# Optimization experiments

Measured on AMD Instinct MI355X. Metric: run time of the kernel, lower is better.

## Reference

```python
import jax, jax.numpy as jnp
import numpy as np

B, S, D = 4, 4096, 768

def setup_inputs() -> dict:
    key = jax.random.key(0)
    k1, k2, k3, k4 = jax.random.split(key, 4)
    x = jax.random.normal(k1, (B, S, D), dtype=jnp.float32)
    # nn.Linear weights: shape [d_out, d_in], applied as x @ W.T
    scale = 1.0 / np.sqrt(D)
    Wq = jax.random.normal(k2, (D, D), dtype=jnp.float32) * scale
    Wk = jax.random.normal(k3, (D, D), dtype=jnp.float32) * scale
    Wv = jax.random.normal(k4, (D, D), dtype=jnp.float32) * scale
    return {"x": x, "Wq": Wq, "Wk": Wk, "Wv": Wv}

def reference(x, Wq, Wk, Wv):
    b, s, d = x.shape
    q = jnp.einsum('bsd,ed->bse', x, Wq)  # Linear: x @ W.T
    k = jnp.einsum('bsd,ed->bse', x, Wk)
    v = jnp.einsum('bsd,ed->bse', x, Wv)
    scores = jnp.einsum('bqe,bke->bqk', q, k)  # [B,S,S]
    causal = jnp.triu(jnp.ones((s, s), dtype=bool), k=1)
    scores = jnp.where(causal, -jnp.inf, scores)
    # original scales by d_out**0.5 (full dim, single head)
    attn = jax.nn.softmax(scores / jnp.sqrt(jnp.asarray(d, x.dtype)), axis=-1)
    return jnp.einsum('bqk,bke->bqe', attn, v)
```

## Files before the change

### kernel.cpp

```cpp
#include <hip/hip_runtime.h>
#include <hip/hip_fp16.h>

typedef unsigned short u16;
typedef unsigned int   u32;
typedef __attribute__((ext_vector_type(8))) _Float16 f16x8;
typedef __attribute__((ext_vector_type(4))) float    f32x4;

#define MFMA(a,b,c) __builtin_amdgcn_mfma_f32_16x16x32_f16(a,b,c,0,0,0)

__device__ __forceinline__ u16 f2h(float f) { return __half_as_ushort(__float2half(f)); }

__device__ __forceinline__ void load_lds16(const void* g, void* l) {
    __builtin_amdgcn_global_load_lds(
        (__attribute__((address_space(1))) void*)g,
        (__attribute__((address_space(3))) void*)l,
        16, 0, 0);
}

__global__ __launch_bounds__(256) void k_conv_x(const float* __restrict__ in, u16* __restrict__ out)
{
    int i = blockIdx.x * 256 + threadIdx.x;
    float4 v = ((const float4*)in)[i];
    ushort4 o; o.x = f2h(v.x); o.y = f2h(v.y); o.z = f2h(v.z); o.w = f2h(v.w);
    ((ushort4*)out)[i] = o;
}

__global__ __launch_bounds__(256) void k_conv_w(const float* __restrict__ w0, const float* __restrict__ w1,
                                                const float* __restrict__ w2, u16* __restrict__ out)
{
    const float* src = (blockIdx.y == 0) ? w0 : (blockIdx.y == 1) ? w1 : w2;
    int i = blockIdx.x * 256 + threadIdx.x;
    float4 v = ((const float4*)src)[i];
    ushort4 o; o.x = f2h(v.x); o.y = f2h(v.y); o.z = f2h(v.z); o.w = f2h(v.w);
    ((ushort4*)(out + (size_t)blockIdx.y * 589824))[i] = o;
}

__global__ __launch_bounds__(256) void k_gemm(const u16* __restrict__ xb, const u16* __restrict__ Wb,
                                              u16* __restrict__ Qw, u16* __restrict__ Kw, u16* __restrict__ Vt)
{
    __shared__ u16 As[2][128*32];
    __shared__ u16 Bs[2][128*32];
    const int tid = threadIdx.x;
    const int l = tid & 63;
    const int wr = tid >> 7, wc = (tid >> 6) & 1;
    const int z = blockIdx.z, bx = blockIdx.x;
    const u16 *Ap, *Bp; u16* Cp; int m0, n0; size_t ldc;
    if (z < 2) { Ap = xb; Bp = Wb + (size_t)z*589824; Cp = (z==0)?Qw:Kw; m0=(bx/6)*128; n0=(bx%6)*128; ldc=768; }
    else       { Ap = Wb + 2*589824; Bp = xb; Cp = Vt; m0=(bx%6)*128; n0=(bx/6)*128; ldc=16384; }

    f32x4 acc[4][4];
    #pragma unroll
    for (int i=0;i<4;++i)
        #pragma unroll
        for (int j=0;j<4;++j) acc[i][j] = (f32x4){0.f,0.f,0.f,0.f};

    const int srow = tid >> 2, sg = tid & 3;
    const int wb = (tid >> 6) << 10;

    #pragma unroll
    for (int i = 0; i < 2; ++i) {
        load_lds16(Ap + (size_t)(m0 + i*64 + srow)*768 + sg*8, (char*)&As[0][0] + i*4096 + wb);
        load_lds16(Bp + (size_t)(n0 + i*64 + srow)*768 + sg*8, (char*)&Bs[0][0] + i*4096 + wb);
    }
    __syncthreads();
    int cur = 0;
    for (int kt = 0; kt < 24; ++kt) {
        if (kt + 1 < 24) {
            const int k0 = (kt+1)*32;
            #pragma unroll
            for (int i = 0; i < 2; ++i) {
                load_lds16(Ap + (size_t)(m0 + i*64 + srow)*768 + k0 + sg*8, (char*)&As[cur^1][0] + i*4096 + wb);
                load_lds16(Bp + (size_t)(n0 + i*64 + srow)*768 + k0 + sg*8, (char*)&Bs[cur^1][0] + i*4096 + wb);
            }
        }
        f16x8 a[4], b[4];
        #pragma unroll
        for (int mi = 0; mi < 4; ++mi) a[mi] = *(const f16x8*)&As[cur][(wr*64 + mi*16 + (l&15))*32 + (l>>4)*8];
        #pragma unroll
        for (int ni = 0; ni < 4; ++ni) b[ni] = *(const f16x8*)&Bs[cur][(wc*64 + ni*16 + (l&15))*32 + (l>>4)*8];
        #pragma unroll
        for (int mi = 0; mi < 4; ++mi)
            #pragma unroll
            for (int ni = 0; ni < 4; ++ni)
                acc[mi][ni] = MFMA(a[mi], b[ni], acc[mi][ni]);
        __syncthreads();
        cur ^= 1;
    }
    const int col = l & 15, rg = (l >> 4) * 4;
    #pragma unroll
    for (int mi = 0; mi < 4; ++mi)
        #pragma unroll
        for (int ni = 0; ni < 4; ++ni)
            #pragma unroll
            for (int j = 0; j < 4; ++j)
                Cp[(size_t)(m0 + wr*64 + mi*16 + rg + j) * ldc + n0 + wc*64 + ni*16 + col] = f2h(acc[mi][ni][j]);
}

#define SM_SCALE 0.03608439182435161f

__global__ __launch_bounds__(1024, 4) void k_flash(const u16* __restrict__ Qg, const u16* __restrict__ Kg,
                                                   const u16* __restrict__ Vtg, float* __restrict__ Og)
{
    __shared__ u16 Qs[32*768];
    __shared__ u16 Ks[32*768];
    __shared__ float Sp[4][32][34];
    __shared__ u16 Ps[32][40];
    __shared__ float row_m[32], row_l[32], row_sc[32];

    const int tid = threadIdx.x;
    const int w = tid >> 6, l = tid & 63;
    const int l15 = l & 15, l4 = l >> 4;
    const int iq = w & 1, jk = (w >> 1) & 1, kh = w >> 2;
    const int dg = w;
    const int batch = blockIdx.x & 3, p = blockIdx.x >> 2;
    const size_t bofs = (size_t)batch * 4096;
    const float NEG_INF = -__builtin_inff();
    const int wbase = w << 10;

    for (int pass = 0; pass < 2; ++pass) {
        const int qi = pass ? p : 127 - p;
        const int q0 = qi * 32;
        const int NT = qi + 1;

        if (tid < 32) { row_m[tid] = NEG_INF; row_l[tid] = 0.f; }

        #pragma unroll
        for (int i = 0; i < 3; ++i) {
            int u = i*1024 + tid, row = u/96, g = u - row*96, gd = g ^ (row & 7);
            load_lds16(Qg + (bofs + q0 + row)*768 + gd*8, (char*)Qs + i*16384 + wbase);
        }
        #pragma unroll
        for (int i = 0; i < 3; ++i) {
            int u = i*1024 + tid, row = u/96, g = u - row*96, gd = g ^ (row & 7);
            load_lds16(Kg + (bofs + row)*768 + gd*8, (char*)Ks + i*16384 + wbase);
        }

        f32x4 oacc[2][3];
        #pragma unroll
        for (int a = 0; a < 2; ++a)
            #pragma unroll
            for (int b = 0; b < 3; ++b) oacc[a][b] = (f32x4){0.f,0.f,0.f,0.f};
        f16x8 vfr[3];

        for (int t = 0; t < NT; ++t) {
            __syncthreads();
            {
                const int qrow = iq*16 + l15, krow = jk*16 + l15;
                const char* qb = (const char*)Qs + qrow*1536;
                const char* kb = (const char*)Ks + krow*1536;
                const int qx = qrow & 7, kx = krow & 7;
                f32x4 s0 = (f32x4){0.f,0.f,0.f,0.f}, s1 = (f32x4){0.f,0.f,0.f,0.f};
                #pragma unroll
                for (int s = 0; s < 6; s += 2) {
                    const int g0 = kh*24 + s*4 + l4, g1 = g0 + 4;
                    f16x8 a0 = *(const f16x8*)(qb + (g0 ^ qx)*16);
                    f16x8 b0 = *(const f16x8*)(kb + (g0 ^ kx)*16);
                    s0 = MFMA(a0, b0, s0);
                    f16x8 a1 = *(const f16x8*)(qb + (g1 ^ qx)*16);
                    f16x8 b1 = *(const f16x8*)(kb + (g1 ^ kx)*16);
                    s1 = MFMA(a1, b1, s1);
                }
                const int sr = iq*16 + l4*4, scc = jk*16 + l15;
                #pragma unroll
                for (int j = 0; j < 4; ++j)
                    Sp[kh][sr + j][scc] = s0[j] + s1[j];
            }
            if (t > 0) {
                const int rb = l4*4;
                #pragma unroll
                for (int qg = 0; qg < 2; ++qg) {
                    const float fr0 = row_sc[qg*16+rb],   fr1 = row_sc[qg*16+rb+1],
                                fr2 = row_sc[qg*16+rb+2], fr3 = row_sc[qg*16+rb+3];
                    f16x8 pa = *(const f16x8*)((const char*)&Ps[0][0] + (qg*16 + l15)*80 + l4*16);
                    #pragma unroll
                    for (int ni = 0; ni < 3; ++ni) {
                        f32x4 o = oacc[qg][ni];
                        o[0]*=fr0; o[1]*=fr1; o[2]*=fr2; o[3]*=fr3;
                        oacc[qg][ni] = MFMA(pa, vfr[ni], o);
                    }
                }
            }
            __syncthreads();
            if (t + 1 < NT) {
                #pragma unroll
                for (int i = 0; i < 3; ++i) {
                    int u = i*1024 + tid, row = u/96, g = u - row*96, gd = g ^ (row & 7);
                    load_lds16(Kg + (bofs + (t+1)*32 + row)*768 + gd*8, (char*)Ks + i*16384 + wbase);
                }
            }
            {
                const u16* vb = Vtg + (size_t)(dg*48 + l15)*16384 + bofs + t*32 + l4*8;
                #pragma unroll
                for (int ni = 0; ni < 3; ++ni)
                    vfr[ni] = *(const f16x8*)(vb + (size_t)ni*262144);
            }
            {
                const int r = tid >> 5, c = tid & 31;
                float a = (Sp[0][r][c] + Sp[1][r][c] + Sp[2][r][c] + Sp[3][r][c]) * SM_SCALE;
                const int qglob = q0 + r, kglob = t*32 + c;
                if (kglob > qglob) a = NEG_INF;
                float mx = a;
                mx = fmaxf(mx, __shfl_xor(mx, 1));
                mx = fmaxf(mx, __shfl_xor(mx, 2));
                mx = fmaxf(mx, __shfl_xor(mx, 4));
                mx = fmaxf(mx, __shfl_xor(mx, 8));
                mx = fmaxf(mx, __shfl_xor(mx, 16));
                const float m_old = row_m[r];
                const float m_new = fmaxf(m_old, mx);
                const float pr = __expf(a - m_new);
                float sum = pr;
                sum += __shfl_xor(sum, 1);
                sum += __shfl_xor(sum, 2);
                sum += __shfl_xor(sum, 4);
                sum += __shfl_xor(sum, 8);
                sum += __shfl_xor(sum, 16);
                const float sc = __expf(m_old - m_new);
                if (c == 0) { row_m[r] = m_new; row_l[r] = row_l[r]*sc + sum; row_sc[r] = sc; }
                Ps[r][c] = f2h(pr);
            }
        }
        __syncthreads();
        {
            const int rb = l4*4;
            #pragma unroll
            for (int qg = 0; qg < 2; ++qg) {
                const float fr0 = row_sc[qg*16+rb],   fr1 = row_sc[qg*16+rb+1],
                            fr2 = row_sc[qg*16+rb+2], fr3 = row_sc[qg*16+rb+3];
                f16x8 pa = *(const f16x8*)((const char*)&Ps[0][0] + (qg*16 + l15)*80 + l4*16);
                #pragma unroll
                for (int ni = 0; ni < 3; ++ni) {
                    f32x4 o = oacc[qg][ni];
                    o[0]*=fr0; o[1]*=fr1; o[2]*=fr2; o[3]*=fr3;
                    oacc[qg][ni] = MFMA(pa, vfr[ni], o);
                }
            }
        }
        {
            const int rb = l4*4;
            #pragma unroll
            for (int qg = 0; qg < 2; ++qg) {
                const float i0 = 1.f/row_l[qg*16+rb],   i1 = 1.f/row_l[qg*16+rb+1],
                            i2 = 1.f/row_l[qg*16+rb+2], i3 = 1.f/row_l[qg*16+rb+3];
                #pragma unroll
                for (int ni = 0; ni < 3; ++ni) {
                    const size_t base = (bofs + q0 + qg*16 + rb) * 768 + dg*48 + ni*16 + l15;
                    Og[base]        = oacc[qg][ni][0] * i0;
                    Og[base + 768]  = oacc[qg][ni][1] * i1;
                    Og[base + 1536] = oacc[qg][ni][2] * i2;
                    Og[base + 2304] = oacc[qg][ni][3] * i3;
                }
            }
        }
        __syncthreads();
    }
}

extern "C" void kernel_launch(void* const* d_in, const int* in_sizes, int n_in,
                              void* d_out, int out_size, void* d_ws, size_t ws_size,
                              hipStream_t stream)
{
    const float* x  = (const float*)d_in[0];
    const float* Wq = (const float*)d_in[1];
    const float* Wk = (const float*)d_in[2];
    const float* Wv = (const float*)d_in[3];
    float* out = (float*)d_out;
    char* ws = (char*)d_ws;
    u16* xb = (u16*)ws;
    u16* Wb = (u16*)(ws + 25165824);
    u16* Qw = (u16*)(ws + 28704768);
    u16* Kw = (u16*)(ws + 53870592);
    u16* Vt = (u16*)(ws + 79036416);

    k_conv_x<<<12288, 256, 0, stream>>>(x, xb);
    k_conv_w<<<dim3(576, 3), 256, 0, stream>>>(Wq, Wk, Wv, Wb);
    k_gemm<<<dim3(768, 1, 3), 256, 0, stream>>>(xb, Wb, Qw, Kw, Vt);
    k_flash<<<256, 1024, 0, stream>>>(Qw, Kw, Vt, out);
}
```

Before: 515.9 us.

## Widen flash attention key tile to 64 and keep Q fragments in registers

Doubles the key/value tile per iteration from 32 to 64 rows, which halves the number of loop iterations and block-wide barriers per query tile. Q is now held in registers, loaded once per pass, instead of being staged in LDS, which frees shared memory for the larger K buffer. The softmax step handles two columns per thread with vectorized LDS reads and writes. The cost is higher register pressure from the Q and doubled V fragments, and more LDS per block, which may reduce occupancy.

```diff
diff --git a/kernel.cpp b/kernel.cpp
--- a/kernel.cpp
+++ b/kernel.cpp
@@ -101,16 +101,15 @@
 __global__ __launch_bounds__(1024, 4) void k_flash(const u16* __restrict__ Qg, const u16* __restrict__ Kg,
                                                    const u16* __restrict__ Vtg, float* __restrict__ Og)
 {
-    __shared__ u16 Qs[32*768];
-    __shared__ u16 Ks[32*768];
-    __shared__ float Sp[4][32][34];
-    __shared__ u16 Ps[32][40];
+    __shared__ u16 Ks[64*768];
+    __shared__ float Sp[4][32][66];
+    __shared__ u16 Ps[32][72];
     __shared__ float row_m[32], row_l[32], row_sc[32];
 
     const int tid = threadIdx.x;
     const int w = tid >> 6, l = tid & 63;
     const int l15 = l & 15, l4 = l >> 4;
-    const int iq = w & 1, jk = (w >> 1) & 1, kh = w >> 2;
+    const int jk = w & 3, kh = w >> 2;
     const int dg = w;
     const int batch = blockIdx.x & 3, p = blockIdx.x >> 2;
     const size_t bofs = (size_t)batch * 4096;
@@ -120,17 +119,21 @@
     for (int pass = 0; pass < 2; ++pass) {
         const int qi = pass ? p : 127 - p;
         const int q0 = qi * 32;
-        const int NT = qi + 1;
+        const int NT = (qi >> 1) + 1;
 
         if (tid < 32) { row_m[tid] = NEG_INF; row_l[tid] = 0.f; }
 
-        #pragma unroll
-        for (int i = 0; i < 3; ++i) {
-            int u = i*1024 + tid, row = u/96, g = u - row*96, gd = g ^ (row & 7);
-            load_lds16(Qg + (bofs + q0 + row)*768 + gd*8, (char*)Qs + i*16384 + wbase);
-        }
-        #pragma unroll
-        for (int i = 0; i < 3; ++i) {
+        f16x8 qf[2][6];
+        {
+            const u16* qb = Qg + (bofs + q0 + l15)*768 + kh*192 + l4*8;
+            #pragma unroll
+            for (int iq = 0; iq < 2; ++iq)
+                #pragma unroll
+                for (int ks = 0; ks < 6; ++ks)
+                    qf[iq][ks] = *(const f16x8*)(qb + iq*12288 + ks*32);
+        }
+        #pragma unroll
+        for (int i = 0; i < 6; ++i) {
             int u = i*1024 + tid, row = u/96, g = u - row*96, gd = g ^ (row & 7);
             load_lds16(Kg + (bofs + row)*768 + gd*8, (char*)Ks + i*16384 + wbase);
         }
@@ -140,30 +143,27 @@
         for (int a = 0; a < 2; ++a)
             #pragma unroll
             for (int b = 0; b < 3; ++b) oacc[a][b] = (f32x4){0.f,0.f,0.f,0.f};
-        f16x8 vfr[3];
+        f16x8 vfr[2][3];
 
         for (int t = 0; t < NT; ++t) {
             __syncthreads();
             {
-                const int qrow = iq*16 + l15, krow = jk*16 + l15;
-                const char* qb = (const char*)Qs + qrow*1536;
-                const char* kb = (const char*)Ks + krow*1536;
-                const int qx = qrow & 7, kx = krow & 7;
+                const char* kb = (const char*)Ks + (jk*16 + l15)*1536;
+                const int kx = l15 & 7;
                 f32x4 s0 = (f32x4){0.f,0.f,0.f,0.f}, s1 = (f32x4){0.f,0.f,0.f,0.f};
                 #pragma unroll
-                for (int s = 0; s < 6; s += 2) {
-                    const int g0 = kh*24 + s*4 + l4, g1 = g0 + 4;
-                    f16x8 a0 = *(const f16x8*)(qb + (g0 ^ qx)*16);
-                    f16x8 b0 = *(const f16x8*)(kb + (g0 ^ kx)*16);
-                    s0 = MFMA(a0, b0, s0);
-                    f16x8 a1 = *(const f16x8*)(qb + (g1 ^ qx)*16);
-                    f16x8 b1 = *(const f16x8*)(kb + (g1 ^ kx)*16);
-                    s1 = MFMA(a1, b1, s1);
-                }
-                const int sr = iq*16 + l4*4, scc = jk*16 + l15;
-                #pragma unroll
-                for (int j = 0; j < 4; ++j)
-                    Sp[kh][sr + j][scc] = s0[j] + s1[j];
+                for (int ks = 0; ks < 6; ++ks) {
+                    const int g = kh*24 + ks*4 + l4;
+                    f16x8 bk = *(const f16x8*)(kb + (g ^ kx)*16);
+                    s0 = MFMA(qf[0][ks], bk, s0);
+                    s1 = MFMA(qf[1][ks], bk, s1);
+                }
+                const int scc = jk*16 + l15, sr = l4*4;
+                #pragma unroll
+                for (int j = 0; j < 4; ++j) {
+                    Sp[kh][sr + j][scc]      = s0[j];
+                    Sp[kh][16 + sr + j][scc] = s1[j];
+                }
             }
             if (t > 0) {
                 const int rb = l4*4;
@@ -171,35 +171,46 @@
                 for (int qg = 0; qg < 2; ++qg) {
                     const float fr0 = row_sc[qg*16+rb],   fr1 = row_sc[qg*16+rb+1],
                                 fr2 = row_sc[qg*16+rb+2], fr3 = row_sc[qg*16+rb+3];
-                    f16x8 pa = *(const f16x8*)((const char*)&Ps[0][0] + (qg*16 + l15)*80 + l4*16);
+                    f16x8 pa0 = *(const f16x8*)((const char*)&Ps[0][0] + (qg*16 + l15)*144 + l4*16);
+                    f16x8 pa1 = *(const f16x8*)((const char*)&Ps[0][0] + (qg*16 + l15)*144 + 64 + l4*16);
                     #pragma unroll
                     for (int ni = 0; ni < 3; ++ni) {
                         f32x4 o = oacc[qg][ni];
                         o[0]*=fr0; o[1]*=fr1; o[2]*=fr2; o[3]*=fr3;
-                        oacc[qg][ni] = MFMA(pa, vfr[ni], o);
+                        o = MFMA(pa0, vfr[0][ni], o);
+                        o = MFMA(pa1, vfr[1][ni], o);
+                        oacc[qg][ni] = o;
                     }
                 }
             }
             __syncthreads();
             if (t + 1 < NT) {
                 #pragma unroll
-                for (int i = 0; i < 3; ++i) {
+                for (int i = 0; i < 6; ++i) {
                     int u = i*1024 + tid, row = u/96, g = u - row*96, gd = g ^ (row & 7);
-                    load_lds16(Kg + (bofs + (t+1)*32 + row)*768 + gd*8, (char*)Ks + i*16384 + wbase);
+                    load_lds16(Kg + (bofs + (t+1)*64 + row)*768 + gd*8, (char*)Ks + i*16384 + wbase);
                 }
             }
             {
-                const u16* vb = Vtg + (size_t)(dg*48 + l15)*16384 + bofs + t*32 + l4*8;
-                #pragma unroll
-                for (int ni = 0; ni < 3; ++ni)
-                    vfr[ni] = *(const f16x8*)(vb + (size_t)ni*262144);
+                const u16* vb = Vtg + (size_t)(dg*48 + l15)*16384 + bofs + t*64 + l4*8;
+                #pragma unroll
+                for (int kt = 0; kt < 2; ++kt)
+                    #pragma unroll
+                    for (int ni = 0; ni < 3; ++ni)
+                        vfr[kt][ni] = *(const f16x8*)(vb + (size_t)ni*262144 + kt*32);
             }
             {
-                const int r = tid >> 5, c = tid & 31;
-                float a = (Sp[0][r][c] + Sp[1][r][c] + Sp[2][r][c] + Sp[3][r][c]) * SM_SCALE;
-                const int qglob = q0 + r, kglob = t*32 + c;
-                if (kglob > qglob) a = NEG_INF;
-                float mx = a;
+                const int r = tid >> 5, c0 = (tid & 31)*2;
+                const float2 v0 = *(const float2*)&Sp[0][r][c0];
+                const float2 v1 = *(const float2*)&Sp[1][r][c0];
+                const float2 v2 = *(const float2*)&Sp[2][r][c0];
+                const float2 v3 = *(const float2*)&Sp[3][r][c0];
+                float a0 = (v0.x + v1.x + v2.x + v3.x) * SM_SCALE;
+                float a1 = (v0.y + v1.y + v2.y + v3.y) * SM_SCALE;
+                const int qglob = q0 + r, kglob = t*64 + c0;
+                if (kglob > qglob)     a0 = NEG_INF;
+                if (kglob + 1 > qglob) a1 = NEG_INF;
+                float mx = fmaxf(a0, a1);
                 mx = fmaxf(mx, __shfl_xor(mx, 1));
                 mx = fmaxf(mx, __shfl_xor(mx, 2));
                 mx = fmaxf(mx, __shfl_xor(mx, 4));
@@ -207,16 +218,18 @@
                 mx = fmaxf(mx, __shfl_xor(mx, 16));
                 const float m_old = row_m[r];
                 const float m_new = fmaxf(m_old, mx);
-                const float pr = __expf(a - m_new);
-                float sum = pr;
+                const float p0 = __expf(a0 - m_new);
+                const float p1 = __expf(a1 - m_new);
+                float sum = p0 + p1;
                 sum += __shfl_xor(sum, 1);
                 sum += __shfl_xor(sum, 2);
                 sum += __shfl_xor(sum, 4);
                 sum += __shfl_xor(sum, 8);
                 sum += __shfl_xor(sum, 16);
                 const float sc = __expf(m_old - m_new);
-                if (c == 0) { row_m[r] = m_new; row_l[r] = row_l[r]*sc + sum; row_sc[r] = sc; }
-                Ps[r][c] = f2h(pr);
+                if ((tid & 31) == 0) { row_m[r] = m_new; row_l[r] = row_l[r]*sc + sum; row_sc[r] = sc; }
+                ushort2 pp; pp.x = f2h(p0); pp.y = f2h(p1);
+                *(ushort2*)&Ps[r][c0] = pp;
             }
         }
         __syncthreads();
@@ -226,12 +239,15 @@
             for (int qg = 0; qg < 2; ++qg) {
                 const float fr0 = row_sc[qg*16+rb],   fr1 = row_sc[qg*16+rb+1],
                             fr2 = row_sc[qg*16+rb+2], fr3 = row_sc[qg*16+rb+3];
-                f16x8 pa = *(const f16x8*)((const char*)&Ps[0][0] + (qg*16 + l15)*80 + l4*16);
+                f16x8 pa0 = *(const f16x8*)((const char*)&Ps[0][0] + (qg*16 + l15)*144 + l4*16);
+                f16x8 pa1 = *(const f16x8*)((const char*)&Ps[0][0] + (qg*16 + l15)*144 + 64 + l4*16);
                 #pragma unroll
                 for (int ni = 0; ni < 3; ++ni) {
                     f32x4 o = oacc[qg][ni];
                     o[0]*=fr0; o[1]*=fr1; o[2]*=fr2; o[3]*=fr3;
-                    oacc[qg][ni] = MFMA(pa, vfr[ni], o);
+                    o = MFMA(pa0, vfr[0][ni], o);
+                    o = MFMA(pa1, vfr[1][ni], o);
+                    oacc[qg][ni] = o;
                 }
             }
         }
```

New measurement: 802.5 us. +55.6%, slower.
